# Kernel tuning notes

Hardware: AMD Instinct MI355X
Metric: run time of the kernel (lower is better)

## Reference

```python
import jax, jax.numpy as jnp
import numpy as np

B, N, E = 16, 10000, 320000
C_IN, C_OUT, K = 32, 64, 3
C = C_IN + C_OUT          # 96, channels into each diffusion conv
L = 2 * K - 1             # 5 Chebyshev terms (bidirectional, remove_ln=False)


def setup_inputs() -> dict:
    key = jax.random.key(0)
    ks = jax.random.split(key, 8)
    x = jax.random.normal(ks[0], (B, N, C_IN), dtype=jnp.float32)
    hidden_state = jax.random.normal(ks[1], (B, N, C_OUT), dtype=jnp.float32)
    edge_index = jax.random.randint(ks[2], (2, E), 0, N, dtype=jnp.int64)
    edge_weight = jax.random.uniform(ks[3], (E,), dtype=jnp.float32)
    # xavier-uniform style scale for params
    s_ru = float(np.sqrt(6.0 / (L * C + 2 * C_OUT)))
    s_c = float(np.sqrt(6.0 / (L * C + C_OUT)))
    ru_param = jax.random.uniform(ks[4], (L * C, 2 * C_OUT), minval=-s_ru, maxval=s_ru, dtype=jnp.float32)
    ru_bias = jnp.zeros((2 * C_OUT,), dtype=jnp.float32)
    c_param = jax.random.uniform(ks[5], (L * C, C_OUT), minval=-s_c, maxval=s_c, dtype=jnp.float32)
    c_bias = jnp.zeros((C_OUT,), dtype=jnp.float32)
    return {"x": x, "hidden_state": hidden_state, "edge_index": edge_index,
            "edge_weight": edge_weight, "ru_param": ru_param, "ru_bias": ru_bias,
            "c_param": c_param, "c_bias": c_bias}


def _propagate(h, src, dst, w, num_nodes):
    # gather x_j at src, weight, scatter-add at dst: out[i] = sum_{e: dst=i} w_e * h[src_e]
    return jax.ops.segment_sum(h[src] * w[:, None], dst, num_segments=num_nodes)


def _cheb_conv(x, src, dst, wf, wb, param, bias, k):
    # x: [B, N, C] -> [N, B*C] as in torch transpose(0,1).view(N, B*C)
    b, n, c = x.shape
    xt = jnp.transpose(x, (1, 0, 2)).reshape(n, b * c)
    x0f = xt
    x0b = xt
    x1f = _propagate(xt, src, dst, wf, n)
    x1b = _propagate(xt, dst, src, wb, n)
    outs = [xt, x1f, x1b]
    for _ in range(2, k):
        x2f = 2.0 * _propagate(x1f, src, dst, wf, n) - x0f
        outs.append(x2f)
        x0f, x1f = x1f, x2f
        x2b = 2.0 * _propagate(x1b, dst, src, wb, n) - x0b
        outs.append(x2b)
        x0b, x1b = x1b, x2b
    out = jnp.stack(outs, axis=2)            # [N, B*C, L]
    out = out.reshape(n * b, -1)             # [N*B, C*L] (row-major matches torch view)
    out = out @ param                        # [N*B, out_channels]
    out = jnp.transpose(out.reshape(n, b, -1), (1, 0, 2))  # [B, N, out]
    return out + bias


def reference(x, hidden_state, edge_index, edge_weight, ru_param, ru_bias, c_param, c_bias):
    src, dst = edge_index[0], edge_index[1]
    n = x.shape[1]
    deg_f = jax.ops.segment_sum(edge_weight, src, num_segments=n)
    wf = edge_weight / deg_f[src]            # forward-diffusion normalized weights
    deg_b = jax.ops.segment_sum(edge_weight, dst, num_segments=n)
    wb = edge_weight / deg_b[dst]            # reverse-diffusion normalized weights

    x_and_state = jnp.concatenate([x, hidden_state], axis=2)
    ru = jax.nn.sigmoid(_cheb_conv(x_and_state, src, dst, wf, wb, ru_param, ru_bias, K))
    r = ru[:, :, :C_OUT]
    u = ru[:, :, C_OUT:]
    xrh = jnp.concatenate([x, r * hidden_state], axis=-1)
    # original applies tanh twice
    c = jnp.tanh(jnp.tanh(_cheb_conv(xrh, src, dst, wf, wb, c_param, c_bias, K)))
    return u * hidden_state + (1.0 - u) * c
```

## Files before the change

kernel.cpp:

```cpp
#include <hip/hip_runtime.h>
#include <stdint.h>
#include <stddef.h>

#define Bn    16
#define Nn    10000
#define En    320000
#define CIN   32
#define COUTn 64
#define CCn   96
#define WROWU 768
#define RHU   512
#define MROWS 160000
#define GX0   (Nn * WROWU / 256)

typedef __attribute__((ext_vector_type(8))) short short8;
typedef __attribute__((ext_vector_type(4))) float f32x4;
typedef __attribute__((ext_vector_type(2))) float f32x2;
typedef __attribute__((ext_vector_type(4))) unsigned int uint4v;

__device__ __forceinline__ float bflo(unsigned int p) { return __uint_as_float(p << 16); }
__device__ __forceinline__ float bfhi(unsigned int p) { return __uint_as_float(p & 0xffff0000u); }
__device__ __forceinline__ float bf2f(unsigned short u) { return __uint_as_float(((unsigned int)u) << 16); }
__device__ __forceinline__ unsigned int f2bfbits(float f) {
  unsigned int x = __float_as_uint(f);
  return (x + 0x7fffu + ((x >> 16) & 1u)) >> 16;
}
__device__ __forceinline__ unsigned int pack2(float lo, float hi) {
  return f2bfbits(lo) | (f2bfbits(hi) << 16);
}

__global__ void detect_idx(const int* __restrict__ idx, int* __restrict__ flag) {
  int t = threadIdx.x;
  int v = idx[1 + 2 * t];
  unsigned long long bal = __ballot(v != 0);
  if (t == 0) flag[0] = (bal == 0ULL) ? 1 : 0;
}

__device__ __forceinline__ int gidx(const int* __restrict__ p, int i, int is64) {
  return is64 ? p[2 * (long long)i] : p[i];
}

__global__ void deg_cnt_kernel(const int* __restrict__ idx, const float* __restrict__ w,
                               float* __restrict__ deg_f, float* __restrict__ deg_b,
                               int* __restrict__ cnt_f, int* __restrict__ cnt_b,
                               const int* __restrict__ flag) {
  int e = blockIdx.x * 256 + threadIdx.x;
  int is64 = flag[0];
  if (e < En) {
    int s = gidx(idx, e, is64);
    int d = gidx(idx, En + e, is64);
    float we = w[e];
    atomicAdd(&deg_f[s], we);
    atomicAdd(&deg_b[d], we);
    atomicAdd(&cnt_f[d], 1);
    atomicAdd(&cnt_b[s], 1);
  }
}

__global__ void exscan_two(const int* __restrict__ cnt_f, const int* __restrict__ cnt_b,
                           int* __restrict__ rp_f, int* __restrict__ rp_b,
                           int* __restrict__ cur_f, int* __restrict__ cur_b, int n) {
  const int* cnt = (blockIdx.x == 0) ? cnt_f : cnt_b;
  int* rp  = (blockIdx.x == 0) ? rp_f  : rp_b;
  int* cur = (blockIdx.x == 0) ? cur_f : cur_b;
  __shared__ int sh[256];
  int t = threadIdx.x;
  int CH = (n + 255) / 256;
  int s0 = t * CH;
  int s1 = s0 + CH; if (s1 > n) s1 = n;
  int s = 0;
  for (int i = s0; i < s1; ++i) s += cnt[i];
  sh[t] = s;
  __syncthreads();
  for (int off = 1; off < 256; off <<= 1) {
    int x = (t >= off) ? sh[t - off] : 0;
    __syncthreads();
    sh[t] += x;
    __syncthreads();
  }
  int run = sh[t] - s;
  for (int i = s0; i < s1; ++i) {
    rp[i] = run; cur[i] = run; run += cnt[i];
  }
  if (t == 255) rp[n] = sh[255];
}

__global__ void fill_csr(const int* __restrict__ idx, const float* __restrict__ w,
                         const float* __restrict__ deg_f, const float* __restrict__ deg_b,
                         int* __restrict__ cur_f, int* __restrict__ cur_b,
                         uint2* __restrict__ cwf, uint2* __restrict__ cwb,
                         const int* __restrict__ flag) {
  int e = blockIdx.x * 256 + threadIdx.x;
  int is64 = flag[0];
  if (e < En) {
    int s = gidx(idx, e, is64);
    int d = gidx(idx, En + e, is64);
    float we = w[e];
    int pf = atomicAdd(&cur_f[d], 1);
    cwf[pf] = make_uint2((unsigned int)s, __float_as_uint(we / deg_f[s]));
    int pb = atomicAdd(&cur_b[s], 1);
    cwb[pb] = make_uint2((unsigned int)d, __float_as_uint(we / deg_b[d]));
  }
}

__global__ void build_x0_wt(const float* __restrict__ x, const float* __restrict__ h,
                            unsigned int* __restrict__ X0,
                            const float* __restrict__ ru_p, const float* __restrict__ c_p,
                            unsigned short* __restrict__ Wt1, unsigned short* __restrict__ Wt2) {
  if (blockIdx.x < GX0) {
    long long p = (long long)blockIdx.x * 256 + threadIdx.x;
    int node = (int)(p / WROWU);
    int rem = (int)(p % WROWU);
    int b = rem / 48;
    int ci = (rem % 48) * 2;
    float lo, hi;
    if (ci < CIN) {
      const float* s = x + ((size_t)b * Nn + node) * CIN + ci;
      lo = s[0]; hi = s[1];
    } else {
      const float* s = h + ((size_t)b * Nn + node) * COUTn + (ci - CIN);
      lo = s[0]; hi = s[1];
    }
    X0[p] = pack2(lo, hi);
  } else {
    int i = (blockIdx.x - GX0) * 256 + threadIdx.x;
    if (i < 128 * 480) {
      int n = i / 480, k = i % 480;
      int t = k / 96, kk = k % 96;
      float v;
      if (t == 0) v = ru_p[(kk * 5 + 0) * 128 + n] - ru_p[(kk * 5 + 3) * 128 + n] - ru_p[(kk * 5 + 4) * 128 + n];
      else        v = ru_p[(kk * 5 + t) * 128 + n];
      Wt1[i] = (unsigned short)f2bfbits(v);
    }
    if (i < 64 * 480) {
      int n = i / 480, k = i % 480;
      int t = k / 96, kk = k % 96;
      float v;
      if (t == 0) v = c_p[(kk * 5 + 0) * 64 + n] - c_p[(kk * 5 + 3) * 64 + n] - c_p[(kk * 5 + 4) * 64 + n];
      else        v = c_p[(kk * 5 + t) * 64 + n];
      Wt2[i] = (unsigned short)f2bfbits(v);
    }
  }
}

template<int RU4, int ACT, int EPW>
__device__ __forceinline__ void prop_rowX(const uint4v* __restrict__ in,
                                          uint4v* __restrict__ out,
                                          const int* __restrict__ rp,
                                          const uint2* __restrict__ cw,
                                          int row, int slice, int lane, float alpha) {
  constexpr int GSZ = 64 / EPW;
  constexpr unsigned RB = (unsigned)RU4 * 16u;
  int grp = (EPW == 2) ? (lane >> 5) : (lane >> 4);
  int lg = lane & (GSZ - 1);
  int lgc = (lg < ACT) ? lg : 0;
  unsigned laneByte = (unsigned)(slice * ACT + lgc) * 16u;
  const char* __restrict__ inB = (const char*)in;
  int jb = __builtin_amdgcn_readfirstlane(rp[row]);
  int je = __builtin_amdgcn_readfirstlane(rp[row + 1]);
  int len = je - jb;

  f32x2 a0 = {0.f, 0.f}, a1 = {0.f, 0.f}, a2 = {0.f, 0.f}, a3 = {0.f, 0.f};

  constexpr int STEP = 4 * EPW;
  int i = jb;
  int eM = jb + (len / STEP) * STEP;
  for (; i < eM; i += STEP) {
    #pragma unroll
    for (int k = 0; k < 4; ++k) {
      unsigned int col; float w;
      {
        uint2 e0 = cw[i + k * EPW + 0];
        uint2 e1 = cw[i + k * EPW + 1];
        col = (grp & 1) ? e1.x : e0.x;
        w = __uint_as_float((grp & 1) ? e1.y : e0.y);
        if (EPW == 4) {
          uint2 e2 = cw[i + k * EPW + 2];
          uint2 e3 = cw[i + k * EPW + 3];
          unsigned int colB = (grp & 1) ? e3.x : e2.x;
          float wB = __uint_as_float((grp & 1) ? e3.y : e2.y);
          col = (grp & 2) ? colB : col;
          w = (grp & 2) ? wB : w;
        }
      }
      unsigned off = __umul24(col, RB) + laneByte;
      uint4v q = *(const uint4v*)(inB + off);
      f32x2 wv = {w, w};
      f32x2 v0 = {bflo(q.x), bfhi(q.x)};
      f32x2 v1 = {bflo(q.y), bfhi(q.y)};
      f32x2 v2 = {bflo(q.z), bfhi(q.z)};
      f32x2 v3 = {bflo(q.w), bfhi(q.w)};
      a0 += wv * v0; a1 += wv * v1; a2 += wv * v2; a3 += wv * v3;
    }
  }
  for (; i < je; i += EPW) {
    unsigned int col; float w;
    {
      uint2 e0 = cw[i + 0];
      uint2 e1 = cw[(i + 1 < je) ? i + 1 : i];
      col = (grp & 1) ? e1.x : e0.x;
      w = __uint_as_float((grp & 1) ? e1.y : e0.y);
      if (EPW == 4) {
        uint2 e2 = cw[(i + 2 < je) ? i + 2 : i];
        uint2 e3 = cw[(i + 3 < je) ? i + 3 : i];
        unsigned int colB = (grp & 1) ? e3.x : e2.x;
        float wB = __uint_as_float((grp & 1) ? e3.y : e2.y);
        col = (grp & 2) ? colB : col;
        w = (grp & 2) ? wB : w;
      }
    }
    if (i + grp >= je) w = 0.f;
    unsigned off = __umul24(col, RB) + laneByte;
    uint4v q = *(const uint4v*)(inB + off);
    f32x2 wv = {w, w};
    f32x2 v0 = {bflo(q.x), bfhi(q.x)};
    f32x2 v1 = {bflo(q.y), bfhi(q.y)};
    f32x2 v2 = {bflo(q.z), bfhi(q.z)};
    f32x2 v3 = {bflo(q.w), bfhi(q.w)};
    a0 += wv * v0; a1 += wv * v1; a2 += wv * v2; a3 += wv * v3;
  }

  if (EPW == 4) {
    a0.x += __shfl_xor(a0.x, 16); a0.y += __shfl_xor(a0.y, 16);
    a1.x += __shfl_xor(a1.x, 16); a1.y += __shfl_xor(a1.y, 16);
    a2.x += __shfl_xor(a2.x, 16); a2.y += __shfl_xor(a2.y, 16);
    a3.x += __shfl_xor(a3.x, 16); a3.y += __shfl_xor(a3.y, 16);
  }
  a0.x += __shfl_xor(a0.x, 32); a0.y += __shfl_xor(a0.y, 32);
  a1.x += __shfl_xor(a1.x, 32); a1.y += __shfl_xor(a1.y, 32);
  a2.x += __shfl_xor(a2.x, 32); a2.y += __shfl_xor(a2.y, 32);
  a3.x += __shfl_xor(a3.x, 32); a3.y += __shfl_xor(a3.y, 32);

  if (grp == 0 && lg < ACT) {
    uint4v o;
    o.x = pack2(alpha * a0.x, alpha * a0.y);
    o.y = pack2(alpha * a1.x, alpha * a1.y);
    o.z = pack2(alpha * a2.x, alpha * a2.y);
    o.w = pack2(alpha * a3.x, alpha * a3.y);
    out[(size_t)row * RU4 + slice * ACT + lg] = o;
  }
}

template<int RU4, int ACT, int EPW>
__launch_bounds__(256)
__global__ void prop_dualX(const uint4v* __restrict__ in,
                           uint4v* __restrict__ outF, uint4v* __restrict__ outB,
                           const int* __restrict__ rp_f, const uint2* __restrict__ cwf,
                           const int* __restrict__ rp_b, const uint2* __restrict__ cwb) {
  int lane = threadIdx.x & 63;
  int wave = threadIdx.x >> 6;
  int slice = blockIdx.x & 7;
  int row = ((blockIdx.x >> 3) << 2) + wave;
  prop_rowX<RU4, ACT, EPW>(in, outF, rp_f, cwf, row, slice, lane, 1.f);
  prop_rowX<RU4, ACT, EPW>(in, outB, rp_b, cwb, row, slice, lane, 1.f);
}

template<int RU4, int ACT, int EPW>
__launch_bounds__(256)
__global__ void prop_ckX(const uint4v* __restrict__ in, uint4v* __restrict__ out,
                         const int* __restrict__ rp, const uint2* __restrict__ cw,
                         float alpha) {
  int lane = threadIdx.x & 63;
  int wave = threadIdx.x >> 6;
  int slice = blockIdx.x & 7;
  int row = ((blockIdx.x >> 3) << 2) + wave;
  prop_rowX<RU4, ACT, EPW>(in, out, rp, cw, row, slice, lane, alpha);
}

struct Msrc {
  const uint4* xs[5];
  const uint4* rh[5];
};

template<int NT, int MODE>
__device__ __forceinline__ void gemm_body(int blk, Msrc g, int nterms, int t0,
                          const unsigned short* __restrict__ Wt,
                          const float* __restrict__ bias,
                          float* __restrict__ outp,
                          unsigned short* __restrict__ rh0_s,
                          unsigned short* __restrict__ U_out,
                          const unsigned short* __restrict__ U_in,
                          const float* __restrict__ hglob) {
  constexpr int NJ = NT / 16;
  __shared__ __align__(16) unsigned short As[128][104];
  __shared__ __align__(16) unsigned short Bs[NT][104];

  int m0 = blk * 128;
  int tid = threadIdx.x;
  int wave = tid >> 6;
  int lane = tid & 63;
  int quad = lane >> 4;
  int lm = lane & 15;
  int wm = wave * 32;
  int nodeBase = m0 >> 4;

  f32x4 acc[2][NJ];
  #pragma unroll
  for (int i = 0; i < 2; ++i)
    #pragma unroll
    for (int j = 0; j < NJ; ++j) acc[i][j] = (f32x4){0.f, 0.f, 0.f, 0.f};

  for (int t = 0; t < nterms; ++t) {
    const uint4* xs4 = g.xs[t];
    const uint4* rh4 = g.rh[t];
    if (rh4 == nullptr) {
      const uint4* src = xs4 + (size_t)m0 * 12;
      #pragma unroll
      for (int it = 0; it < 6; ++it) {
        int q = tid + it * 256;
        uint4 v = src[q];
        int row = q / 12, slot = q % 12;
        *(uint4*)&As[row][slot * 8] = v;
      }
    } else {
      #pragma unroll
      for (int it = 0; it < 6; ++it) {
        int q = tid + it * 256;
        int row = q / 12, slot = q % 12;
        int node = nodeBase + (row >> 4);
        int b = row & 15;
        uint4 v; int ci0;
        if (slot < 4) { v = xs4[(size_t)node * 192 + b * 12 + slot]; ci0 = slot * 8; }
        else          { v = rh4[(size_t)node * 128 + b * 8 + (slot - 4)]; ci0 = 32 + (slot - 4) * 8; }
        *(uint4*)&As[row][ci0] = v;
      }
    }
    for (int q = tid; q < NT * 12; q += 256) {
      int n = q / 12, slot = q % 12;
      uint4 v = *(const uint4*)(Wt + (size_t)n * 480 + (t0 + t) * 96 + slot * 8);
      *(uint4*)&Bs[n][slot * 8] = v;
    }
    __syncthreads();

    #pragma unroll
    for (int k32 = 0; k32 < 3; ++k32) {
      int kb = k32 * 32 + quad * 8;
      short8 a0 = *(const short8*)&As[wm + lm][kb];
      short8 a1 = *(const short8*)&As[wm + 16 + lm][kb];
      #pragma unroll
      for (int j = 0; j < NJ; ++j) {
        short8 bf = *(const short8*)&Bs[j * 16 + lm][kb];
        acc[0][j] = __builtin_amdgcn_mfma_f32_16x16x32_bf16(a0, bf, acc[0][j], 0, 0, 0);
        acc[1][j] = __builtin_amdgcn_mfma_f32_16x16x32_bf16(a1, bf, acc[1][j], 0, 0, 0);
      }
    }
    __syncthreads();
  }

  #pragma unroll
  for (int i = 0; i < 2; ++i) {
    #pragma unroll
    for (int j = 0; j < NJ; ++j) {
      int col = j * 16 + lm;
      #pragma unroll
      for (int r = 0; r < 4; ++r) {
        int row = m0 + wm + i * 16 + quad * 4 + r;
        int node = row >> 4, b = row & 15;
        float v = acc[i][j][r];
        if (MODE == 0) {
          float s = 1.f / (1.f + expf(-(bias[col] + v)));
          if (col < COUTn) {
            float hv = hglob[((size_t)b * Nn + node) * COUTn + col];
            rh0_s[(size_t)row * 64 + col] = (unsigned short)f2bfbits(s * hv);
          } else {
            U_out[(size_t)row * 64 + (col - COUTn)] = (unsigned short)f2bfbits(s);
          }
        } else if (MODE == 1) {
          outp[((size_t)b * Nn + node) * COUTn + col] = bias[col] + v;
        } else {
          size_t oa = ((size_t)b * Nn + node) * COUTn + col;
          float cp = outp[oa] + v;
          float c = tanhf(tanhf(cp));
          float u = bf2f(U_in[(size_t)row * 64 + col]);
          outp[oa] = u * hglob[oa] + (1.f - u) * c;
        }
      }
    }
  }
}

template<int NT, int MODE>
__launch_bounds__(256)
__global__ void gemm_mfma(Msrc g, int nterms, int t0,
                          const unsigned short* __restrict__ Wt,
                          const float* __restrict__ bias,
                          float* __restrict__ outp,
                          unsigned short* __restrict__ rh0_s,
                          unsigned short* __restrict__ U_out,
                          const unsigned short* __restrict__ U_in,
                          const float* __restrict__ hglob) {
  gemm_body<NT, MODE>(blockIdx.x, g, nterms, t0, Wt, bias, outp, rh0_s, U_out, U_in, hglob);
}

__launch_bounds__(256)
__global__ void fused_g2a(Msrc g,
                          const unsigned short* __restrict__ Wt,
                          const float* __restrict__ bias,
                          float* __restrict__ outp,
                          const uint4v* __restrict__ inF, uint4v* __restrict__ outF,
                          const int* __restrict__ rp_f, const uint2* __restrict__ cwf,
                          const uint4v* __restrict__ inB, uint4v* __restrict__ outB,
                          const int* __restrict__ rp_b, const uint2* __restrict__ cwb) {
  int b = blockIdx.x;
  if (b < 1256) {
    if (b < 1250)
      gemm_body<64, 1>(b, g, 3, 0, Wt, bias, outp, nullptr, nullptr, nullptr, nullptr);
    return;
  }
  int lane = threadIdx.x & 63;
  int wave = threadIdx.x >> 6;
  if (b < 21256) {
    int b2 = b - 1256;
    prop_rowX<128, 16, 4>(inF, outF, rp_f, cwf, ((b2 >> 3) << 2) + wave, b2 & 7, lane, 2.f);
  } else {
    int b2 = b - 21256;
    prop_rowX<128, 16, 4>(inB, outB, rp_b, cwb, ((b2 >> 3) << 2) + wave, b2 & 7, lane, 2.f);
  }
}

extern "C" void kernel_launch(void* const* d_in, const int* in_sizes, int n_in,
                              void* d_out, int out_size, void* d_ws, size_t ws_size,
                              hipStream_t stream) {
  const float* x   = (const float*)d_in[0];
  const float* h   = (const float*)d_in[1];
  const int*   idx = (const int*)d_in[2];
  const float* ew  = (const float*)d_in[3];
  const float* ru_param = (const float*)d_in[4];
  const float* ru_bias  = (const float*)d_in[5];
  const float* c_param  = (const float*)d_in[6];
  const float* c_bias   = (const float*)d_in[7];
  float* outp = (float*)d_out;
  (void)in_sizes; (void)n_in; (void)out_size;

  char* ws = (char*)d_ws;
  size_t off = 0;
  auto alloc = [&](size_t bytes) -> char* {
    char* p = ws + off;
    off += (bytes + 255) & ~(size_t)255;
    return p;
  };

  float* deg_f = (float*)alloc(40960);
  float* deg_b = (float*)alloc(40960);
  int*   cnt_f = (int*)alloc(40960);
  int*   cnt_b = (int*)alloc(40960);
  int*   rp_f  = (int*)alloc((Nn + 1) * sizeof(int));
  int*   rp_b  = (int*)alloc((Nn + 1) * sizeof(int));
  int*   cur_f = (int*)alloc(Nn * sizeof(int));
  int*   cur_b = (int*)alloc(Nn * sizeof(int));
  int*   flag  = (int*)alloc(256);
  uint2* cwf   = (uint2*)alloc((size_t)En * 8);
  uint2* cwb   = (uint2*)alloc((size_t)En * 8);
  unsigned short* Wt1 = (unsigned short*)alloc(128 * 480 * 2);
  unsigned short* Wt2 = (unsigned short*)alloc(64 * 480 * 2);

  unsigned int* A0   = (unsigned int*)alloc((size_t)Nn * WROWU * 4);
  unsigned int* T1f  = (unsigned int*)alloc((size_t)Nn * WROWU * 4);
  unsigned int* T1b  = (unsigned int*)alloc((size_t)Nn * WROWU * 4);
  unsigned int* T2f  = (unsigned int*)alloc((size_t)Nn * WROWU * 4);
  unsigned int* T2b  = (unsigned int*)alloc((size_t)Nn * WROWU * 4);
  unsigned int* rh0  = (unsigned int*)alloc((size_t)Nn * RHU * 4);
  unsigned int* rh1f = (unsigned int*)alloc((size_t)Nn * RHU * 4);
  unsigned int* rh1b = (unsigned int*)alloc((size_t)Nn * RHU * 4);
  unsigned int* Ubuf = (unsigned int*)alloc((size_t)Nn * RHU * 4);
  unsigned int* rh2fN = (unsigned int*)alloc((size_t)Nn * RHU * 4);
  unsigned int* rh2bN = (unsigned int*)alloc((size_t)Nn * RHU * 4);
  bool bigws = (off <= ws_size);

  hipMemsetAsync(ws, 0, 4 * 40960, stream);
  detect_idx<<<1, 64, 0, stream>>>(idx, flag);
  deg_cnt_kernel<<<En / 256, 256, 0, stream>>>(idx, ew, deg_f, deg_b, cnt_f, cnt_b, flag);
  exscan_two<<<2, 256, 0, stream>>>(cnt_f, cnt_b, rp_f, rp_b, cur_f, cur_b, Nn);
  fill_csr<<<En / 256, 256, 0, stream>>>(idx, ew, deg_f, deg_b, cur_f, cur_b,
                                         cwf, cwb, flag);
  build_x0_wt<<<GX0 + 240, 256, 0, stream>>>(x, h, A0, ru_param, c_param, Wt1, Wt2);

  const int gP = (Nn / 4) * 8;

  prop_dualX<192, 24, 2><<<gP, 256, 0, stream>>>(
      (const uint4v*)A0, (uint4v*)T1f, (uint4v*)T1b, rp_f, cwf, rp_b, cwb);
  prop_ckX<192, 24, 2><<<gP, 256, 0, stream>>>(
      (const uint4v*)T1f, (uint4v*)T2f, rp_f, cwf, 2.f);
  prop_ckX<192, 24, 2><<<gP, 256, 0, stream>>>(
      (const uint4v*)T1b, (uint4v*)T2b, rp_b, cwb, 2.f);

  Msrc g1;
  g1.xs[0] = (const uint4*)A0;  g1.rh[0] = nullptr;
  g1.xs[1] = (const uint4*)T1f; g1.rh[1] = nullptr;
  g1.xs[2] = (const uint4*)T1b; g1.rh[2] = nullptr;
  g1.xs[3] = (const uint4*)T2f; g1.rh[3] = nullptr;
  g1.xs[4] = (const uint4*)T2b; g1.rh[4] = nullptr;
  gemm_mfma<128, 0><<<MROWS / 128, 256, 0, stream>>>(
      g1, 5, 0, Wt1, ru_bias, nullptr,
      (unsigned short*)rh0, (unsigned short*)Ubuf, nullptr, h);

  prop_dualX<128, 16, 4><<<gP, 256, 0, stream>>>(
      (const uint4v*)rh0, (uint4v*)rh1f, (uint4v*)rh1b, rp_f, cwf, rp_b, cwb);

  Msrc g2a;
  g2a.xs[0] = (const uint4*)A0;  g2a.rh[0] = (const uint4*)rh0;
  g2a.xs[1] = (const uint4*)T1f; g2a.rh[1] = (const uint4*)rh1f;
  g2a.xs[2] = (const uint4*)T1b; g2a.rh[2] = (const uint4*)rh1b;
  g2a.xs[3] = nullptr; g2a.rh[3] = nullptr;
  g2a.xs[4] = nullptr; g2a.rh[4] = nullptr;

  const uint4* g2b_rh0;
  const uint4* g2b_rh1;
  if (bigws) {
    fused_g2a<<<41256, 256, 0, stream>>>(
        g2a, Wt2, c_bias, outp,
        (const uint4v*)rh1f, (uint4v*)rh2fN, rp_f, cwf,
        (const uint4v*)rh1b, (uint4v*)rh2bN, rp_b, cwb);
    g2b_rh0 = (const uint4*)rh2fN;
    g2b_rh1 = (const uint4*)rh2bN;
  } else {
    gemm_mfma<64, 1><<<MROWS / 128, 256, 0, stream>>>(
        g2a, 3, 0, Wt2, c_bias, outp, nullptr, nullptr, nullptr, nullptr);
    prop_ckX<128, 16, 4><<<gP, 256, 0, stream>>>(
        (const uint4v*)rh1f, (uint4v*)rh0, rp_f, cwf, 2.f);
    prop_ckX<128, 16, 4><<<gP, 256, 0, stream>>>(
        (const uint4v*)rh1b, (uint4v*)rh1f, rp_b, cwb, 2.f);
    g2b_rh0 = (const uint4*)rh0;
    g2b_rh1 = (const uint4*)rh1f;
  }

  Msrc g2b;
  g2b.xs[0] = (const uint4*)T2f; g2b.rh[0] = g2b_rh0;
  g2b.xs[1] = (const uint4*)T2b; g2b.rh[1] = g2b_rh1;
  g2b.xs[2] = nullptr; g2b.rh[2] = nullptr;
  g2b.xs[3] = nullptr; g2b.rh[3] = nullptr;
  g2b.xs[4] = nullptr; g2b.rh[4] = nullptr;
  gemm_mfma<64, 2><<<MROWS / 128, 256, 0, stream>>>(
      g2b, 2, 3, Wt2, c_bias, outp, nullptr, nullptr,
      (const unsigned short*)Ubuf, h);
}
```

Measured before the change: 852.0 us.

## Merge degree/x0/weight prep kernels and use direct global-to-LDS loads in GEMM

Merges the degree-count kernel with the x0/weight build kernel into a single launch, removing one kernel launch and letting the independent work share the GPU. In the GEMM, the padded LDS tiles become unpadded 96-wide rows so that the global_load_lds builtin can copy tiles from global memory straight into LDS without going through registers. Dropping the padding can raise LDS bank conflicts on the MFMA operand reads. The direct-to-LDS path is used only when the builtin is available.

```diff
diff --git a/kernel.cpp b/kernel.cpp
--- a/kernel.cpp
+++ b/kernel.cpp
@@ -11,12 +11,24 @@
 #define WROWU 768
 #define RHU   512
 #define MROWS 160000
+#define GDEG  (En / 256)
 #define GX0   (Nn * WROWU / 256)
 
 typedef __attribute__((ext_vector_type(8))) short short8;
 typedef __attribute__((ext_vector_type(4))) float f32x4;
 typedef __attribute__((ext_vector_type(2))) float f32x2;
 typedef __attribute__((ext_vector_type(4))) unsigned int uint4v;
+
+#if __has_builtin(__builtin_amdgcn_global_load_lds)
+#define HAVE_GLL 1
+typedef __attribute__((address_space(3))) unsigned char lds_u8;
+typedef __attribute__((address_space(1))) const unsigned char glb_u8;
+__device__ __forceinline__ void gll16(const void* g, void* l) {
+  __builtin_amdgcn_global_load_lds((glb_u8*)g, (lds_u8*)l, 16, 0, 0);
+}
+#else
+#define HAVE_GLL 0
+#endif
 
 __device__ __forceinline__ float bflo(unsigned int p) { return __uint_as_float(p << 16); }
 __device__ __forceinline__ float bfhi(unsigned int p) { return __uint_as_float(p & 0xffff0000u); }
@@ -40,20 +52,60 @@
   return is64 ? p[2 * (long long)i] : p[i];
 }
 
-__global__ void deg_cnt_kernel(const int* __restrict__ idx, const float* __restrict__ w,
-                               float* __restrict__ deg_f, float* __restrict__ deg_b,
-                               int* __restrict__ cnt_f, int* __restrict__ cnt_b,
-                               const int* __restrict__ flag) {
-  int e = blockIdx.x * 256 + threadIdx.x;
-  int is64 = flag[0];
-  if (e < En) {
-    int s = gidx(idx, e, is64);
-    int d = gidx(idx, En + e, is64);
-    float we = w[e];
-    atomicAdd(&deg_f[s], we);
-    atomicAdd(&deg_b[d], we);
-    atomicAdd(&cnt_f[d], 1);
-    atomicAdd(&cnt_b[s], 1);
+__global__ void deg_x0_wt(const int* __restrict__ idx, const float* __restrict__ w,
+                          float* __restrict__ deg_f, float* __restrict__ deg_b,
+                          int* __restrict__ cnt_f, int* __restrict__ cnt_b,
+                          const int* __restrict__ flag,
+                          const float* __restrict__ x, const float* __restrict__ h,
+                          unsigned int* __restrict__ X0,
+                          const float* __restrict__ ru_p, const float* __restrict__ c_p,
+                          unsigned short* __restrict__ Wt1, unsigned short* __restrict__ Wt2) {
+  int blk = blockIdx.x;
+  if (blk < GDEG) {
+    int e = blk * 256 + threadIdx.x;
+    int is64 = flag[0];
+    if (e < En) {
+      int s = gidx(idx, e, is64);
+      int d = gidx(idx, En + e, is64);
+      float we = w[e];
+      atomicAdd(&deg_f[s], we);
+      atomicAdd(&deg_b[d], we);
+      atomicAdd(&cnt_f[d], 1);
+      atomicAdd(&cnt_b[s], 1);
+    }
+  } else if (blk < GDEG + GX0) {
+    long long p = (long long)(blk - GDEG) * 256 + threadIdx.x;
+    int node = (int)(p / WROWU);
+    int rem = (int)(p % WROWU);
+    int b = rem / 48;
+    int ci = (rem % 48) * 2;
+    float lo, hi;
+    if (ci < CIN) {
+      const float* s = x + ((size_t)b * Nn + node) * CIN + ci;
+      lo = s[0]; hi = s[1];
+    } else {
+      const float* s = h + ((size_t)b * Nn + node) * COUTn + (ci - CIN);
+      lo = s[0]; hi = s[1];
+    }
+    X0[p] = pack2(lo, hi);
+  } else {
+    int i = (blk - GDEG - GX0) * 256 + threadIdx.x;
+    if (i < 128 * 480) {
+      int n = i / 480, k = i % 480;
+      int t = k / 96, kk = k % 96;
+      float v;
+      if (t == 0) v = ru_p[(kk * 5 + 0) * 128 + n] - ru_p[(kk * 5 + 3) * 128 + n] - ru_p[(kk * 5 + 4) * 128 + n];
+      else        v = ru_p[(kk * 5 + t) * 128 + n];
+      Wt1[i] = (unsigned short)f2bfbits(v);
+    }
+    if (i < 64 * 480) {
+      int n = i / 480, k = i % 480;
+      int t = k / 96, kk = k % 96;
+      float v;
+      if (t == 0) v = c_p[(kk * 5 + 0) * 64 + n] - c_p[(kk * 5 + 3) * 64 + n] - c_p[(kk * 5 + 4) * 64 + n];
+      else        v = c_p[(kk * 5 + t) * 64 + n];
+      Wt2[i] = (unsigned short)f2bfbits(v);
+    }
   }
 }
 
@@ -103,46 +155,6 @@
   }
 }
 
-__global__ void build_x0_wt(const float* __restrict__ x, const float* __restrict__ h,
-                            unsigned int* __restrict__ X0,
-                            const float* __restrict__ ru_p, const float* __restrict__ c_p,
-                            unsigned short* __restrict__ Wt1, unsigned short* __restrict__ Wt2) {
-  if (blockIdx.x < GX0) {
-    long long p = (long long)blockIdx.x * 256 + threadIdx.x;
-    int node = (int)(p / WROWU);
-    int rem = (int)(p % WROWU);
-    int b = rem / 48;
-    int ci = (rem % 48) * 2;
-    float lo, hi;
-    if (ci < CIN) {
-      const float* s = x + ((size_t)b * Nn + node) * CIN + ci;
-      lo = s[0]; hi = s[1];
-    } else {
-      const float* s = h + ((size_t)b * Nn + node) * COUTn + (ci - CIN);
-      lo = s[0]; hi = s[1];
-    }
-    X0[p] = pack2(lo, hi);
-  } else {
-    int i = (blockIdx.x - GX0) * 256 + threadIdx.x;
-    if (i < 128 * 480) {
-      int n = i / 480, k = i % 480;
-      int t = k / 96, kk = k % 96;
-      float v;
-      if (t == 0) v = ru_p[(kk * 5 + 0) * 128 + n] - ru_p[(kk * 5 + 3) * 128 + n] - ru_p[(kk * 5 + 4) * 128 + n];
-      else        v = ru_p[(kk * 5 + t) * 128 + n];
-      Wt1[i] = (unsigned short)f2bfbits(v);
-    }
-    if (i < 64 * 480) {
-      int n = i / 480, k = i % 480;
-      int t = k / 96, kk = k % 96;
-      float v;
-      if (t == 0) v = c_p[(kk * 5 + 0) * 64 + n] - c_p[(kk * 5 + 3) * 64 + n] - c_p[(kk * 5 + 4) * 64 + n];
-      else        v = c_p[(kk * 5 + t) * 64 + n];
-      Wt2[i] = (unsigned short)f2bfbits(v);
-    }
-  }
-}
-
 template<int RU4, int ACT, int EPW>
 __device__ __forceinline__ void prop_rowX(const uint4v* __restrict__ in,
                                           uint4v* __restrict__ out,
@@ -282,8 +294,8 @@
                           const unsigned short* __restrict__ U_in,
                           const float* __restrict__ hglob) {
   constexpr int NJ = NT / 16;
-  __shared__ __align__(16) unsigned short As[128][104];
-  __shared__ __align__(16) unsigned short Bs[NT][104];
+  __shared__ __align__(16) unsigned short As[128 * 96];
+  __shared__ __align__(16) unsigned short Bs[NT * 96];
 
   int m0 = blk * 128;
   int tid = threadIdx.x;
@@ -305,13 +317,20 @@
     const uint4* rh4 = g.rh[t];
     if (rh4 == nullptr) {
       const uint4* src = xs4 + (size_t)m0 * 12;
+#if HAVE_GLL
+      #pragma unroll
+      for (int it = 0; it < 6; ++it) {
+        int q = tid + it * 256;
+        gll16(src + q, (char*)As + (q & ~63) * 16);
+      }
+#else
       #pragma unroll
       for (int it = 0; it < 6; ++it) {
         int q = tid + it * 256;
         uint4 v = src[q];
-        int row = q / 12, slot = q % 12;
-        *(uint4*)&As[row][slot * 8] = v;
-      }
+        *(uint4*)&As[q * 8] = v;
+      }
+#endif
     } else {
       #pragma unroll
       for (int it = 0; it < 6; ++it) {
@@ -319,27 +338,36 @@
         int row = q / 12, slot = q % 12;
         int node = nodeBase + (row >> 4);
         int b = row & 15;
-        uint4 v; int ci0;
-        if (slot < 4) { v = xs4[(size_t)node * 192 + b * 12 + slot]; ci0 = slot * 8; }
-        else          { v = rh4[(size_t)node * 128 + b * 8 + (slot - 4)]; ci0 = 32 + (slot - 4) * 8; }
-        *(uint4*)&As[row][ci0] = v;
-      }
-    }
+        uint4 v;
+        if (slot < 4) v = xs4[(size_t)node * 192 + b * 12 + slot];
+        else          v = rh4[(size_t)node * 128 + b * 8 + (slot - 4)];
+        *(uint4*)&As[q * 8] = v;
+      }
+    }
+#if HAVE_GLL
+    #pragma unroll
+    for (int it = 0; it < NT * 12 / 256; ++it) {
+      int q = tid + it * 256;
+      int n = q / 12, slot = q % 12;
+      gll16(Wt + (size_t)n * 480 + (t0 + t) * 96 + slot * 8, (char*)Bs + (q & ~63) * 16);
+    }
+#else
     for (int q = tid; q < NT * 12; q += 256) {
       int n = q / 12, slot = q % 12;
       uint4 v = *(const uint4*)(Wt + (size_t)n * 480 + (t0 + t) * 96 + slot * 8);
-      *(uint4*)&Bs[n][slot * 8] = v;
-    }
+      *(uint4*)&Bs[q * 8] = v;
+    }
+#endif
     __syncthreads();
 
     #pragma unroll
     for (int k32 = 0; k32 < 3; ++k32) {
       int kb = k32 * 32 + quad * 8;
-      short8 a0 = *(const short8*)&As[wm + lm][kb];
-      short8 a1 = *(const short8*)&As[wm + 16 + lm][kb];
+      short8 a0 = *(const short8*)&As[(wm + lm) * 96 + kb];
+      short8 a1 = *(const short8*)&As[(wm + 16 + lm) * 96 + kb];
       #pragma unroll
       for (int j = 0; j < NJ; ++j) {
-        short8 bf = *(const short8*)&Bs[j * 16 + lm][kb];
+        short8 bf = *(const short8*)&Bs[(j * 16 + lm) * 96 + kb];
         acc[0][j] = __builtin_amdgcn_mfma_f32_16x16x32_bf16(a0, bf, acc[0][j], 0, 0, 0);
         acc[1][j] = __builtin_amdgcn_mfma_f32_16x16x32_bf16(a1, bf, acc[1][j], 0, 0, 0);
       }
@@ -469,11 +497,12 @@
 
   hipMemsetAsync(ws, 0, 4 * 40960, stream);
   detect_idx<<<1, 64, 0, stream>>>(idx, flag);
-  deg_cnt_kernel<<<En / 256, 256, 0, stream>>>(idx, ew, deg_f, deg_b, cnt_f, cnt_b, flag);
+  deg_x0_wt<<<GDEG + GX0 + 240, 256, 0, stream>>>(
+      idx, ew, deg_f, deg_b, cnt_f, cnt_b, flag,
+      x, h, A0, ru_param, c_param, Wt1, Wt2);
   exscan_two<<<2, 256, 0, stream>>>(cnt_f, cnt_b, rp_f, rp_b, cur_f, cur_b, Nn);
   fill_csr<<<En / 256, 256, 0, stream>>>(idx, ew, deg_f, deg_b, cur_f, cur_b,
                                          cwf, cwb, flag);
-  build_x0_wt<<<GX0 + 240, 256, 0, stream>>>(x, h, A0, ru_param, c_param, Wt1, Wt2);
 
   const int gP = (Nn / 4) * 8;
 
```

Result: faster. 811.5 us (-4.8%).
